# Optimization experiments

Hardware: AMD Instinct MI355X
Metric: run time of the kernel (lower is better)

Reference implementation:

```python
import jax, jax.numpy as jnp
import numpy as np

N_NODES = 100000
N_EDGES = 1600000
IN_SIZE = 256
OUT_SIZE = 64


def setup_inputs() -> dict:
    key = jax.random.key(0)
    k1, k2, k3 = jax.random.split(key, 3)
    edge_index = jax.random.randint(k1, (2, N_EDGES), 0, N_NODES, dtype=jnp.int32)
    x = jax.random.normal(k2, (N_NODES, IN_SIZE), dtype=jnp.float32)
    W = jax.random.normal(k3, (OUT_SIZE, IN_SIZE), dtype=jnp.float32) * 0.05
    return {"edge_index": edge_index, "x": x, "num_nodes": N_NODES, "W": W}


def reference(edge_index, x, num_nodes, W):
    row, col = edge_index[0], edge_index[1]
    # fill_diag(adj, 1.0): drop any existing diagonal entries (value -> 0),
    # then add exactly one self-loop per node with value 1.0.
    val = jnp.where(row == col, 0.0, 1.0).astype(x.dtype)
    loops = jnp.arange(num_nodes, dtype=row.dtype)
    row_f = jnp.concatenate([row, loops])
    col_f = jnp.concatenate([col, loops])
    val_f = jnp.concatenate([val, jnp.ones((num_nodes,), dtype=x.dtype)])
    # deg = row-sum of adjacency values; D^{-1/2} with inf -> 0
    deg = jax.ops.segment_sum(val_f, row_f, num_segments=num_nodes)
    dinv = jnp.where(deg > 0, deg ** -0.5, 0.0)
    # edge weight: d^{-1/2}[row] * a * d^{-1/2}[col]
    norm = dinv[row_f] * val_f * dinv[col_f]
    # dense projection then SpMM aggregation
    xw = x @ W.T  # [N, out]
    msgs = norm[:, None] * xw[col_f]  # gather over edges [E+N, out]
    out = jax.ops.segment_sum(msgs, row_f, num_segments=num_nodes)
    return out
```

## Files before the change

kernel.cpp:

```cpp
#include <hip/hip_runtime.h>

#define IN_SIZE 256
#define OUT_SIZE 64
#define CAP 10240
#define K1_TILE 4096

typedef __attribute__((ext_vector_type(8))) short short8;
typedef __attribute__((ext_vector_type(4))) float floatx4;

__device__ inline unsigned short f2bf(float f) {
  unsigned u = __builtin_bit_cast(unsigned, f);
  u += 0x7fff + ((u >> 16) & 1);
  return (unsigned short)(u >> 16);
}
__device__ inline float bf2f(unsigned short u) {
  unsigned v = (unsigned)u << 16;
  return __builtin_bit_cast(float, v);
}

__global__ __launch_bounds__(256) void bucket_coarse_kernel(
    const int* __restrict__ row, const int* __restrict__ col,
    int* __restrict__ coarse_cursor, unsigned* __restrict__ pairs,
    int n_edges, int nbuck) {
  __shared__ int hist[256];
  int tid = threadIdx.x;
  hist[tid] = 0;
  __syncthreads();

  int r[16], c[16];
  int ebase = blockIdx.x * K1_TILE + tid;
#pragma unroll
  for (int i = 0; i < 16; i++) {
    int e = ebase + i * 256;
    bool ok = e < n_edges;
    r[i] = ok ? row[e] : -1;
    c[i] = ok ? col[e] : -1;
    if (ok && r[i] != c[i]) atomicAdd(&hist[r[i] >> 9], 1);
  }
  __syncthreads();

  if (tid < nbuck) {
    int cnt = hist[tid];
    hist[tid] = atomicAdd(&coarse_cursor[tid], cnt);
  }
  __syncthreads();

#pragma unroll
  for (int i = 0; i < 16; i++) {
    if (r[i] >= 0 && r[i] != c[i]) {
      int bin = r[i] >> 9;
      int slot = atomicAdd(&hist[bin], 1);
      if (slot < CAP)
        pairs[(size_t)bin * CAP + slot] =
            ((unsigned)(r[i] & 511) << 17) | (unsigned)c[i];
    }
  }
}

__global__ __launch_bounds__(256) void bucket_fine_kernel(
    const int* __restrict__ coarse_cursor, const unsigned* __restrict__ pairs,
    unsigned* __restrict__ colsp, int* __restrict__ count,
    int* __restrict__ row_start, float* __restrict__ dinv, int n_nodes) {
  __shared__ int hist[512];
  __shared__ int ssum[256];
  int tid = threadIdx.x;
  int b = blockIdx.x;
  size_t base = (size_t)b * CAP;
  int n_b = coarse_cursor[b];
  if (n_b > CAP) n_b = CAP;

  hist[tid] = 0;
  hist[tid + 256] = 0;
  __syncthreads();

  for (int i = tid; i < n_b; i += 256)
    atomicAdd(&hist[pairs[base + i] >> 17], 1);
  __syncthreads();

  int v0 = hist[2 * tid], v1 = hist[2 * tid + 1];
  ssum[tid] = v0 + v1;
  __syncthreads();
  for (int off = 1; off < 256; off <<= 1) {
    int t = (tid >= off) ? ssum[tid - off] : 0;
    __syncthreads();
    ssum[tid] += t;
    __syncthreads();
  }
  int e0 = (tid > 0) ? ssum[tid - 1] : 0;
  int e1 = e0 + v0;

  {
    int r0 = b * 512 + 2 * tid;
    if (r0 < n_nodes) {
      count[r0] = v0;
      row_start[r0] = (int)base + e0;
      dinv[r0] = rsqrtf((float)v0 + 1.0f);
    }
    int r1 = r0 + 1;
    if (r1 < n_nodes) {
      count[r1] = v1;
      row_start[r1] = (int)base + e1;
      dinv[r1] = rsqrtf((float)v1 + 1.0f);
    }
  }
  hist[2 * tid] = e0;
  hist[2 * tid + 1] = e1;
  __syncthreads();

  for (int i = tid; i < n_b; i += 256) {
    unsigned p = pairs[base + i];
    int slot = atomicAdd(&hist[p >> 17], 1);
    colsp[base + slot] = p & 0x1FFFFu;
  }
}

#define WPAD 264
#define XPAD 136
__global__ __launch_bounds__(256) void matmul_kernel(const float* __restrict__ x,
                                                     const float* __restrict__ W,
                                                     const float* __restrict__ dinv,
                                                     unsigned short* __restrict__ xwd,
                                                     int n_nodes) {
  __shared__ unsigned short w_lds[64][WPAD];
  __shared__ unsigned short x_lds[64][XPAD];

  int tid = threadIdx.x;
  int wave = tid >> 6;
  int lane = tid & 63;
  int quad = lane >> 4;
  int lcol = lane & 15;
  long nbase = (long)blockIdx.x * 64;

  {
    int r = tid >> 2;
    int q = tid & 3;
    const float* src = W + (size_t)r * IN_SIZE;
#pragma unroll
    for (int i = 0; i < 8; i++) {
      int c = q * 64 + i * 8;
      float4 a = *(const float4*)(src + c);
      float4 bb = *(const float4*)(src + c + 4);
      short8 v;
      v[0] = (short)f2bf(a.x); v[1] = (short)f2bf(a.y);
      v[2] = (short)f2bf(a.z); v[3] = (short)f2bf(a.w);
      v[4] = (short)f2bf(bb.x); v[5] = (short)f2bf(bb.y);
      v[6] = (short)f2bf(bb.z); v[7] = (short)f2bf(bb.w);
      *(short8*)(&w_lds[r][c]) = v;
    }
  }

  floatx4 acc[4];
#pragma unroll
  for (int t = 0; t < 4; t++) acc[t] = (floatx4){0.f, 0.f, 0.f, 0.f};

  for (int h = 0; h < 2; h++) {
    {
      int r = tid >> 2;
      int q = tid & 3;
      long node = nbase + r;
      const float* src = x + node * IN_SIZE + h * 128 + q * 32;
      bool ok = (node < (long)n_nodes);
#pragma unroll
      for (int i = 0; i < 4; i++) {
        float4 a = ok ? *(const float4*)(src + i * 8)
                      : make_float4(0.f, 0.f, 0.f, 0.f);
        float4 bb = ok ? *(const float4*)(src + i * 8 + 4)
                       : make_float4(0.f, 0.f, 0.f, 0.f);
        short8 v;
        v[0] = (short)f2bf(a.x); v[1] = (short)f2bf(a.y);
        v[2] = (short)f2bf(a.z); v[3] = (short)f2bf(a.w);
        v[4] = (short)f2bf(bb.x); v[5] = (short)f2bf(bb.y);
        v[6] = (short)f2bf(bb.z); v[7] = (short)f2bf(bb.w);
        *(short8*)(&x_lds[r][q * 32 + i * 8]) = v;
      }
    }
    __syncthreads();

#pragma unroll
    for (int kk = 0; kk < 4; kk++) {
      short8 bfrag = *(const short8*)(&x_lds[wave * 16 + lcol][kk * 32 + quad * 8]);
#pragma unroll
      for (int t = 0; t < 4; t++) {
        short8 afrag = *(const short8*)(
            &w_lds[t * 16 + lcol][h * 128 + kk * 32 + quad * 8]);
        acc[t] =
            __builtin_amdgcn_mfma_f32_16x16x32_bf16(afrag, bfrag, acc[t], 0, 0, 0);
      }
    }
    __syncthreads();
  }

  long node = nbase + wave * 16 + lcol;
  if (node < (long)n_nodes) {
    float dv = dinv[node];
#pragma unroll
    for (int t = 0; t < 4; t++) {
      ushort4 sv;
      sv.x = f2bf(dv * acc[t][0]);
      sv.y = f2bf(dv * acc[t][1]);
      sv.z = f2bf(dv * acc[t][2]);
      sv.w = f2bf(dv * acc[t][3]);
      *(ushort4*)(xwd + node * OUT_SIZE + t * 16 + quad * 4) = sv;
    }
  }
}

__global__ __launch_bounds__(256) void gather_kernel(const int* __restrict__ row_start,
                                                     const int* __restrict__ count,
                                                     const unsigned* __restrict__ colsp,
                                                     const float* __restrict__ dinv,
                                                     const unsigned short* __restrict__ xwd,
                                                     float* __restrict__ out,
                                                     int n_nodes) {
  int lane = threadIdx.x & 63;
  int r = blockIdx.x * 4 + (threadIdx.x >> 6);
  if (r >= n_nodes) return;
  int sub = lane >> 4;
  int cg = lane & 15;
  int start = row_start[r];
  int cnt = count[r];

  float a0 = 0.f, a1 = 0.f, a2 = 0.f, a3 = 0.f;
  if (sub == 0) {
    ushort4 v = *(const ushort4*)(xwd + (size_t)r * OUT_SIZE + cg * 4);
    a0 = bf2f(v.x); a1 = bf2f(v.y); a2 = bf2f(v.z); a3 = bf2f(v.w);
  }
  for (int j = 0; j < cnt; j += 4) {
    int idx = j + sub;
    bool act = idx < cnt;
    int c = act ? (int)colsp[start + idx] : r;
    ushort4 v = *(const ushort4*)(xwd + (size_t)c * OUT_SIZE + cg * 4);
    float m = act ? 1.0f : 0.0f;
    a0 += m * bf2f(v.x);
    a1 += m * bf2f(v.y);
    a2 += m * bf2f(v.z);
    a3 += m * bf2f(v.w);
  }
  a0 += __shfl_xor(a0, 16); a0 += __shfl_xor(a0, 32);
  a1 += __shfl_xor(a1, 16); a1 += __shfl_xor(a1, 32);
  a2 += __shfl_xor(a2, 16); a2 += __shfl_xor(a2, 32);
  a3 += __shfl_xor(a3, 16); a3 += __shfl_xor(a3, 32);

  if (sub == 0) {
    float dr = dinv[r];
    float4 o = make_float4(dr * a0, dr * a1, dr * a2, dr * a3);
    *(float4*)(out + (size_t)r * OUT_SIZE + cg * 4) = o;
  }
}

extern "C" void kernel_launch(void* const* d_in, const int* in_sizes, int n_in,
                              void* d_out, int out_size, void* d_ws,
                              size_t ws_size, hipStream_t stream) {
  const int* edge_index = (const int*)d_in[0];
  const float* x = (const float*)d_in[1];
  const float* W = (const float*)d_in[3];

  int n_edges = in_sizes[0] / 2;
  int n_nodes = in_sizes[1] / IN_SIZE;
  const int* row = edge_index;
  const int* col = edge_index + n_edges;
  float* out = (float*)d_out;

  int nbuck = (n_nodes + 511) >> 9;

  char* ws = (char*)d_ws;
  size_t nb = ((size_t)n_nodes * 4 + 15) & ~(size_t)15;
  int* count = (int*)ws;
  int* row_start = (int*)(ws + nb);
  float* dinv = (float*)(ws + 2 * nb);
  int* coarse_cursor = (int*)(ws + 3 * nb);
  size_t bucketsB = (size_t)nbuck * CAP * 4;
  unsigned* pairs = (unsigned*)(ws + 3 * nb + 4096);
  unsigned* colsp = (unsigned*)(ws + 3 * nb + 4096 + bucketsB);
  unsigned short* xwd =
      (unsigned short*)(ws + 3 * nb + 4096 + 2 * bucketsB);

  hipMemsetAsync(coarse_cursor, 0, (size_t)nbuck * 4, stream);

  int nb1 = (n_edges + K1_TILE - 1) / K1_TILE;
  bucket_coarse_kernel<<<nb1, 256, 0, stream>>>(row, col, coarse_cursor,
                                                pairs, n_edges, nbuck);
  bucket_fine_kernel<<<nbuck, 256, 0, stream>>>(coarse_cursor, pairs, colsp,
                                                count, row_start, dinv,
                                                n_nodes);
  matmul_kernel<<<(n_nodes + 63) / 64, 256, 0, stream>>>(x, W, dinv, xwd,
                                                         n_nodes);
  gather_kernel<<<(n_nodes + 3) / 4, 256, 0, stream>>>(
      row_start, count, colsp, dinv, xwd, out, n_nodes);
}
```

Before: 288.1 us.

## Pre-convert W to bf16, load x fragments directly, widen gather loads

Adds a small kernel that converts W to bf16 once, so each matmul block copies bf16 W into LDS instead of converting fp32 per block. The matmul now loads x rows from global memory straight into MFMA B fragments, which removes the x LDS staging and the two barriers per half. The gather kernel uses 16-byte short8 loads, with 8 lanes per column group and 8 edges per iteration, cutting the number of load instructions per edge. The risks are less coalesced x loads, since each lane reads its own row in 32-byte pieces, and one extra kernel launch.

```diff
diff --git a/kernel.cpp b/kernel.cpp
--- a/kernel.cpp
+++ b/kernel.cpp
@@ -16,6 +16,13 @@
 __device__ inline float bf2f(unsigned short u) {
   unsigned v = (unsigned)u << 16;
   return __builtin_bit_cast(float, v);
+}
+
+__global__ __launch_bounds__(256) void wconv_kernel(const float* __restrict__ W,
+                                                    unsigned short* __restrict__ Wb,
+                                                    int total) {
+  int i = blockIdx.x * 256 + threadIdx.x;
+  if (i < total) Wb[i] = f2bf(W[i]);
 }
 
 __global__ __launch_bounds__(256) void bucket_coarse_kernel(
@@ -115,14 +122,11 @@
 }
 
 #define WPAD 264
-#define XPAD 136
-__global__ __launch_bounds__(256) void matmul_kernel(const float* __restrict__ x,
-                                                     const float* __restrict__ W,
-                                                     const float* __restrict__ dinv,
-                                                     unsigned short* __restrict__ xwd,
-                                                     int n_nodes) {
+__global__ __launch_bounds__(256) void matmul_kernel(
+    const float* __restrict__ x, const unsigned short* __restrict__ Wb,
+    const float* __restrict__ dinv, unsigned short* __restrict__ xwd,
+    int n_nodes) {
   __shared__ unsigned short w_lds[64][WPAD];
-  __shared__ unsigned short x_lds[64][XPAD];
 
   int tid = threadIdx.x;
   int wave = tid >> 6;
@@ -134,63 +138,39 @@
   {
     int r = tid >> 2;
     int q = tid & 3;
-    const float* src = W + (size_t)r * IN_SIZE;
-#pragma unroll
-    for (int i = 0; i < 8; i++) {
-      int c = q * 64 + i * 8;
-      float4 a = *(const float4*)(src + c);
-      float4 bb = *(const float4*)(src + c + 4);
-      short8 v;
-      v[0] = (short)f2bf(a.x); v[1] = (short)f2bf(a.y);
-      v[2] = (short)f2bf(a.z); v[3] = (short)f2bf(a.w);
-      v[4] = (short)f2bf(bb.x); v[5] = (short)f2bf(bb.y);
-      v[6] = (short)f2bf(bb.z); v[7] = (short)f2bf(bb.w);
-      *(short8*)(&w_lds[r][c]) = v;
-    }
-  }
+    const unsigned short* src = Wb + (size_t)r * IN_SIZE + q * 64;
+#pragma unroll
+    for (int i = 0; i < 8; i++)
+      *(short8*)(&w_lds[r][q * 64 + i * 8]) = *(const short8*)(src + i * 8);
+  }
+  __syncthreads();
+
+  long node = nbase + wave * 16 + lcol;
+  long nclamp = (node < (long)n_nodes) ? node : (long)(n_nodes - 1);
+  const float* xrow = x + nclamp * IN_SIZE;
 
   floatx4 acc[4];
 #pragma unroll
   for (int t = 0; t < 4; t++) acc[t] = (floatx4){0.f, 0.f, 0.f, 0.f};
 
-  for (int h = 0; h < 2; h++) {
-    {
-      int r = tid >> 2;
-      int q = tid & 3;
-      long node = nbase + r;
-      const float* src = x + node * IN_SIZE + h * 128 + q * 32;
-      bool ok = (node < (long)n_nodes);
-#pragma unroll
-      for (int i = 0; i < 4; i++) {
-        float4 a = ok ? *(const float4*)(src + i * 8)
-                      : make_float4(0.f, 0.f, 0.f, 0.f);
-        float4 bb = ok ? *(const float4*)(src + i * 8 + 4)
-                       : make_float4(0.f, 0.f, 0.f, 0.f);
-        short8 v;
-        v[0] = (short)f2bf(a.x); v[1] = (short)f2bf(a.y);
-        v[2] = (short)f2bf(a.z); v[3] = (short)f2bf(a.w);
-        v[4] = (short)f2bf(bb.x); v[5] = (short)f2bf(bb.y);
-        v[6] = (short)f2bf(bb.z); v[7] = (short)f2bf(bb.w);
-        *(short8*)(&x_lds[r][q * 32 + i * 8]) = v;
-      }
-    }
-    __syncthreads();
-
-#pragma unroll
-    for (int kk = 0; kk < 4; kk++) {
-      short8 bfrag = *(const short8*)(&x_lds[wave * 16 + lcol][kk * 32 + quad * 8]);
-#pragma unroll
-      for (int t = 0; t < 4; t++) {
-        short8 afrag = *(const short8*)(
-            &w_lds[t * 16 + lcol][h * 128 + kk * 32 + quad * 8]);
-        acc[t] =
-            __builtin_amdgcn_mfma_f32_16x16x32_bf16(afrag, bfrag, acc[t], 0, 0, 0);
-      }
-    }
-    __syncthreads();
-  }
-
-  long node = nbase + wave * 16 + lcol;
+#pragma unroll
+  for (int kk = 0; kk < 8; kk++) {
+    const float* p = xrow + kk * 32 + quad * 8;
+    float4 a = *(const float4*)(p);
+    float4 bb = *(const float4*)(p + 4);
+    short8 bfrag;
+    bfrag[0] = (short)f2bf(a.x);  bfrag[1] = (short)f2bf(a.y);
+    bfrag[2] = (short)f2bf(a.z);  bfrag[3] = (short)f2bf(a.w);
+    bfrag[4] = (short)f2bf(bb.x); bfrag[5] = (short)f2bf(bb.y);
+    bfrag[6] = (short)f2bf(bb.z); bfrag[7] = (short)f2bf(bb.w);
+#pragma unroll
+    for (int t = 0; t < 4; t++) {
+      short8 afrag = *(const short8*)(&w_lds[t * 16 + lcol][kk * 32 + quad * 8]);
+      acc[t] =
+          __builtin_amdgcn_mfma_f32_16x16x32_bf16(afrag, bfrag, acc[t], 0, 0, 0);
+    }
+  }
+
   if (node < (long)n_nodes) {
     float dv = dinv[node];
 #pragma unroll
@@ -205,46 +185,51 @@
   }
 }
 
-__global__ __launch_bounds__(256) void gather_kernel(const int* __restrict__ row_start,
-                                                     const int* __restrict__ count,
-                                                     const unsigned* __restrict__ colsp,
-                                                     const float* __restrict__ dinv,
-                                                     const unsigned short* __restrict__ xwd,
-                                                     float* __restrict__ out,
-                                                     int n_nodes) {
+__global__ __launch_bounds__(256) void gather_kernel(
+    const int* __restrict__ row_start, const int* __restrict__ count,
+    const unsigned* __restrict__ colsp, const float* __restrict__ dinv,
+    const unsigned short* __restrict__ xwd, float* __restrict__ out,
+    int n_nodes) {
   int lane = threadIdx.x & 63;
   int r = blockIdx.x * 4 + (threadIdx.x >> 6);
   if (r >= n_nodes) return;
-  int sub = lane >> 4;
-  int cg = lane & 15;
+  int sub = lane & 7;
+  int cg = lane >> 3;
   int start = row_start[r];
   int cnt = count[r];
 
-  float a0 = 0.f, a1 = 0.f, a2 = 0.f, a3 = 0.f;
+  float acc[8];
+#pragma unroll
+  for (int i = 0; i < 8; i++) acc[i] = 0.f;
+
   if (sub == 0) {
-    ushort4 v = *(const ushort4*)(xwd + (size_t)r * OUT_SIZE + cg * 4);
-    a0 = bf2f(v.x); a1 = bf2f(v.y); a2 = bf2f(v.z); a3 = bf2f(v.w);
-  }
-  for (int j = 0; j < cnt; j += 4) {
+    short8 v = *(const short8*)(xwd + (size_t)r * OUT_SIZE + cg * 8);
+#pragma unroll
+    for (int i = 0; i < 8; i++) acc[i] = bf2f((unsigned short)v[i]);
+  }
+  for (int j = 0; j < cnt; j += 8) {
     int idx = j + sub;
     bool act = idx < cnt;
     int c = act ? (int)colsp[start + idx] : r;
-    ushort4 v = *(const ushort4*)(xwd + (size_t)c * OUT_SIZE + cg * 4);
+    short8 v = *(const short8*)(xwd + (size_t)c * OUT_SIZE + cg * 8);
     float m = act ? 1.0f : 0.0f;
-    a0 += m * bf2f(v.x);
-    a1 += m * bf2f(v.y);
-    a2 += m * bf2f(v.z);
-    a3 += m * bf2f(v.w);
-  }
-  a0 += __shfl_xor(a0, 16); a0 += __shfl_xor(a0, 32);
-  a1 += __shfl_xor(a1, 16); a1 += __shfl_xor(a1, 32);
-  a2 += __shfl_xor(a2, 16); a2 += __shfl_xor(a2, 32);
-  a3 += __shfl_xor(a3, 16); a3 += __shfl_xor(a3, 32);
+#pragma unroll
+    for (int i = 0; i < 8; i++) acc[i] += m * bf2f((unsigned short)v[i]);
+  }
+#pragma unroll
+  for (int i = 0; i < 8; i++) {
+    acc[i] += __shfl_xor(acc[i], 1);
+    acc[i] += __shfl_xor(acc[i], 2);
+    acc[i] += __shfl_xor(acc[i], 4);
+  }
 
   if (sub == 0) {
     float dr = dinv[r];
-    float4 o = make_float4(dr * a0, dr * a1, dr * a2, dr * a3);
-    *(float4*)(out + (size_t)r * OUT_SIZE + cg * 4) = o;
+    float4 o0 = make_float4(dr * acc[0], dr * acc[1], dr * acc[2], dr * acc[3]);
+    float4 o1 = make_float4(dr * acc[4], dr * acc[5], dr * acc[6], dr * acc[7]);
+    float* dst = out + (size_t)r * OUT_SIZE + cg * 8;
+    *(float4*)(dst) = o0;
+    *(float4*)(dst + 4) = o1;
   }
 }
 
@@ -272,18 +257,22 @@
   size_t bucketsB = (size_t)nbuck * CAP * 4;
   unsigned* pairs = (unsigned*)(ws + 3 * nb + 4096);
   unsigned* colsp = (unsigned*)(ws + 3 * nb + 4096 + bucketsB);
-  unsigned short* xwd =
-      (unsigned short*)(ws + 3 * nb + 4096 + 2 * bucketsB);
+  unsigned short* xwd = (unsigned short*)(ws + 3 * nb + 4096 + 2 * bucketsB);
+  unsigned short* Wb =
+      (unsigned short*)(ws + 3 * nb + 4096 + 2 * bucketsB +
+                        (size_t)n_nodes * OUT_SIZE * 2);
 
   hipMemsetAsync(coarse_cursor, 0, (size_t)nbuck * 4, stream);
 
+  wconv_kernel<<<(OUT_SIZE * IN_SIZE + 255) / 256, 256, 0, stream>>>(
+      W, Wb, OUT_SIZE * IN_SIZE);
   int nb1 = (n_edges + K1_TILE - 1) / K1_TILE;
   bucket_coarse_kernel<<<nb1, 256, 0, stream>>>(row, col, coarse_cursor,
                                                 pairs, n_edges, nbuck);
   bucket_fine_kernel<<<nbuck, 256, 0, stream>>>(coarse_cursor, pairs, colsp,
                                                 count, row_start, dinv,
                                                 n_nodes);
-  matmul_kernel<<<(n_nodes + 63) / 64, 256, 0, stream>>>(x, W, dinv, xwd,
+  matmul_kernel<<<(n_nodes + 63) / 64, 256, 0, stream>>>(x, Wb, dinv, xwd,
                                                          n_nodes);
   gather_kernel<<<(n_nodes + 3) / 4, 256, 0, stream>>>(
       row_start, count, colsp, dinv, xwd, out, n_nodes);
```

Result: faster. 278.3 us (-3.4%).
